# Kernel optimization log

Measured on AMD Instinct MI355X. Metric: run time of the kernel, lower is better.

Reference implementation:

```python
import jax, jax.numpy as jnp
import numpy as np

DIM = 1024
EXPAND = 2
HEAD_DIM = 64
D_STATE = 128
N_GROUPS = 1
D_CONV = 4
D_INNER = DIM * EXPAND            # 2048
N_HEADS = D_INNER // HEAD_DIM     # 32
CONV_DIM = D_INNER + 2 * N_GROUPS * D_STATE  # 2304
D_IN_PROJ = 2 * D_INNER + 2 * N_GROUPS * D_STATE + N_HEADS  # 4384
SEQLEN = 4096
LN_EPS = 1e-5


def setup_inputs() -> dict:
    key = jax.random.key(0)
    ks = jax.random.split(key, 6)
    x = jax.random.normal(ks[0], (SEQLEN, DIM), dtype=jnp.float32)
    W_in = jax.random.normal(ks[1], (D_IN_PROJ, DIM), dtype=jnp.float32) * 0.02
    conv_w = jax.random.normal(ks[2], (CONV_DIM, 1, D_CONV), dtype=jnp.float32) * 0.2
    conv_b = jax.random.normal(ks[3], (CONV_DIM,), dtype=jnp.float32) * 0.02
    # dt_bias init per module: dt ~ exp(U*(log(dt_max)-log(dt_min))+log(dt_min)); inv-softplus
    u = jax.random.uniform(ks[4], (N_HEADS,))
    dt = jnp.exp(u * (np.log(0.1) - np.log(0.001)) + np.log(0.001))
    dt = jnp.clip(dt, 1e-4)
    dt_bias = dt + jnp.log(-jnp.expm1(-dt))
    A_log = jnp.log(jax.random.uniform(ks[5], (N_HEADS,), minval=1.0, maxval=16.0))
    D = jnp.ones((N_HEADS,), dtype=jnp.float32)
    ln_w = jnp.ones((D_INNER,), dtype=jnp.float32)
    ln_b = jnp.zeros((D_INNER,), dtype=jnp.float32)
    W_out = jax.random.normal(jax.random.fold_in(key, 7), (DIM, D_INNER), dtype=jnp.float32) * 0.02
    return {"x": x, "W_in": W_in, "conv_w": conv_w, "conv_b": conv_b,
            "dt_bias": dt_bias, "A_log": A_log, "D": D,
            "ln_w": ln_w, "ln_b": ln_b, "W_out": W_out}


def _forward(x, W_in, conv_w, conv_b, dt_bias, A_log, D, ln_w, ln_b, W_out):
    L = x.shape[0]
    dtype = x.dtype
    A = -jnp.exp(A_log.astype(jnp.float32))  # (h,)
    zxbcdt = x @ W_in.T                       # (L, d_in_proj)
    z = zxbcdt[:, :D_INNER]                   # (L, d_inner)
    xbc = zxbcdt[:, D_INNER:D_INNER + CONV_DIM]
    dt = zxbcdt[:, -N_HEADS:]
    dt = jax.nn.softplus(dt.astype(jnp.float32) + dt_bias.astype(jnp.float32))  # (L, h)
    # depthwise 1D conv, SAME padding (module uses padding='SAME', then slices to L)
    xbc_c = jax.lax.conv_general_dilated(
        xbc.T[None],                          # (1, conv_dim, L)
        conv_w,                               # (conv_dim, 1, k)
        window_strides=(1,), padding='SAME',
        dimension_numbers=('NCH', 'OIH', 'NCH'),
        feature_group_count=CONV_DIM,
    )[0].T + conv_b                           # (L, conv_dim)
    xbc_s = jax.nn.silu(xbc_c)
    x_in = xbc_s[:, :D_INNER].reshape(L, N_HEADS, HEAD_DIM)      # (L, h, p)
    B = xbc_s[:, D_INNER:D_INNER + N_GROUPS * D_STATE]          # (L, n) with g=1
    C = xbc_s[:, D_INNER + N_GROUPS * D_STATE:]                 # (L, n)
    # non-causal linear attention (VSSD): y = C (B^T (x * dt * A)) + x * D
    dA = dt.astype(dtype) * A.astype(dtype)                     # (L, h)
    Vs = x_in * dA[..., None]                                   # (L, h, p)
    KV = jnp.einsum('ln,lhp->hnp', B, Vs)                       # (h, n, p)
    y = jnp.einsum('ln,hnp->lhp', C, KV) + x_in * D[None, :, None]
    y = y.reshape(L, D_INNER)
    # per-token LayerNorm, then multiplicative SiLU(z) gate
    mu = jnp.mean(y, axis=-1, keepdims=True)
    var = jnp.var(y, axis=-1, keepdims=True)
    yn = (y - mu) * jax.lax.rsqrt(var + LN_EPS) * ln_w + ln_b
    y = yn * jax.nn.silu(z)
    return y @ W_out.T                                          # (L, dim)


def reference(x, W_in, conv_w, conv_b, dt_bias, A_log, D, ln_w, ln_b, W_out):
    return _forward(x, W_in, conv_w, conv_b, dt_bias, A_log, D, ln_w, ln_b, W_out)
```

## Files before the change

### kernel.cpp

```cpp
#include <hip/hip_runtime.h>
#include <math.h>

#define SEQLEN    4096
#define DIM_IN    1024
#define D_INNER   2048
#define N_HEADS   32
#define D_STATE   128
#define CONV_DIM  2304
#define D_IN_PROJ 4384
#define PROJ_LD   4480
#define LN_EPS    1e-5f
#define KV_SPLIT  16

typedef __attribute__((ext_vector_type(8))) short bf16x8;
typedef __attribute__((ext_vector_type(4))) float f32x4;
typedef __attribute__((ext_vector_type(8))) short short8;

__device__ __forceinline__ ushort f2bf(float f) {
    union { float f; unsigned u; } v; v.f = f;
    unsigned u = v.u + 0x7FFFu + ((v.u >> 16) & 1u);
    return (ushort)(u >> 16);
}
__device__ __forceinline__ float bf2f(ushort h) {
    union { unsigned u; float f; } v; v.u = ((unsigned)h) << 16;
    return v.f;
}

__device__ __forceinline__ void gload16(const void* g, void* l) {
    __builtin_amdgcn_global_load_lds(
        (const __attribute__((address_space(1))) void*)g,
        (__attribute__((address_space(3))) void*)l, 16, 0, 0);
}

#define XB_GROUPS   (SEQLEN * DIM_IN / 8)
#define WIN_GROUPS  (PROJ_LD * DIM_IN / 8)
#define WOUT_GROUPS (DIM_IN * D_INNER / 8)
__global__ __launch_bounds__(256)
void cvt_all(const float* __restrict__ x, const float* __restrict__ W_in,
             const float* __restrict__ W_out,
             ushort* __restrict__ xb, ushort* __restrict__ Winb,
             ushort* __restrict__ Woutb) {
    int i = blockIdx.x * 256 + threadIdx.x;
    const float* src;
    ushort* dst;
    int gi;
    if (i < XB_GROUPS) {
        src = x; dst = xb; gi = i;
    } else if (i < XB_GROUPS + WIN_GROUPS) {
        gi = i - XB_GROUPS;
        int row = (gi * 8) >> 10;
        if (row >= D_IN_PROJ) {
            *reinterpret_cast<short8*>(&Winb[(size_t)gi * 8]) = (short8){0,0,0,0,0,0,0,0};
            return;
        }
        src = W_in; dst = Winb;
    } else if (i < XB_GROUPS + WIN_GROUPS + WOUT_GROUPS) {
        gi = i - (XB_GROUPS + WIN_GROUPS);
        src = W_out; dst = Woutb;
    } else return;
    float4 v0 = reinterpret_cast<const float4*>(src)[gi * 2];
    float4 v1 = reinterpret_cast<const float4*>(src)[gi * 2 + 1];
    short8 r;
    r[0] = f2bf(v0.x); r[1] = f2bf(v0.y); r[2] = f2bf(v0.z); r[3] = f2bf(v0.w);
    r[4] = f2bf(v1.x); r[5] = f2bf(v1.y); r[6] = f2bf(v1.z); r[7] = f2bf(v1.w);
    *reinterpret_cast<short8*>(&dst[(size_t)gi * 8]) = r;
}
#define CVT_TOTAL (XB_GROUPS + WIN_GROUPS + WOUT_GROUPS)

template<int NT, int NTB>
__global__ __launch_bounds__(256, 2)
void gemm_bf16_big(const ushort* __restrict__ A, int lda,
                   const ushort* __restrict__ B, int ldb,
                   ushort* __restrict__ Cout, int ldc) {
    __shared__ __align__(16) ushort S[3][12288];

    const int nwg = gridDim.x;
    const int wg  = blockIdx.x;
    const int swz = (wg & 7) * (nwg >> 3) + (wg >> 3);
    const int m0 = (swz / NTB) * 256;
    const int n0 = (swz % NTB) * 128;

    const int tid  = threadIdx.x;
    const int wave = tid >> 6;
    const int lane = tid & 63;
    const int wm = (wave >> 1) * 128;
    const int wn = (wave & 1) * 64;
    const int r16 = lane & 15;
    const int kg  = lane >> 4;
    const int pkg = kg ^ ((r16 >> 1) & 3);

    f32x4 acc[8][4];
    #pragma unroll
    for (int i = 0; i < 8; ++i)
        #pragma unroll
        for (int j = 0; j < 4; ++j) acc[i][j] = (f32x4){0.f, 0.f, 0.f, 0.f};

    const int srow = lane >> 2;
    const int scol = ((lane & 3) ^ ((lane >> 3) & 3)) * 8;
    const ushort* gsrc[6];
    #pragma unroll
    for (int i = 0; i < 6; ++i) {
        int c = wave * 6 + i;
        gsrc[i] = (c < 16)
            ? A + (size_t)(m0 + c * 16 + srow) * lda + scol
            : B + (size_t)(n0 + (c - 16) * 16 + srow) * ldb + scol;
    }

#define STAGE_BIG(T, BUF)                                            \
    {                                                                \
        const int _k = (T) * 32;                                     \
        _Pragma("unroll")                                            \
        for (int i = 0; i < 6; ++i)                                  \
            gload16(gsrc[i] + _k, &S[BUF][(wave * 6 + i) * 512]);    \
    }

    STAGE_BIG(0, 0)
    STAGE_BIG(1, 1)

    int rb = 0;
    for (int t = 0; t < NT; ++t) {
        __builtin_amdgcn_sched_barrier(0);
        if (t + 1 < NT) {
            asm volatile("s_waitcnt vmcnt(6)" ::: "memory");
        } else {
            asm volatile("s_waitcnt vmcnt(0)" ::: "memory");
        }
        __builtin_amdgcn_s_barrier();
        __builtin_amdgcn_sched_barrier(0);

        if (t + 2 < NT) {
            int sb = rb + 2; if (sb >= 3) sb -= 3;
            STAGE_BIG(t + 2, sb)
        }

        const ushort* sp = &S[rb][0];
        bf16x8 b4[4];
        #pragma unroll
        for (int ni = 0; ni < 4; ++ni)
            b4[ni] = *reinterpret_cast<const bf16x8*>(
                &sp[8192 + (wn + ni * 16 + r16) * 32 + pkg * 8]);
        #pragma unroll
        for (int mh = 0; mh < 2; ++mh) {
            bf16x8 a4[4];
            #pragma unroll
            for (int i = 0; i < 4; ++i)
                a4[i] = *reinterpret_cast<const bf16x8*>(
                    &sp[(wm + (mh * 4 + i) * 16 + r16) * 32 + pkg * 8]);
            __builtin_amdgcn_s_setprio(1);
            #pragma unroll
            for (int i = 0; i < 4; ++i)
                #pragma unroll
                for (int ni = 0; ni < 4; ++ni)
                    acc[mh * 4 + i][ni] = __builtin_amdgcn_mfma_f32_16x16x32_bf16(
                        a4[i], b4[ni], acc[mh * 4 + i][ni], 0, 0, 0);
            __builtin_amdgcn_s_setprio(0);
        }
        rb = (rb == 2) ? 0 : rb + 1;
    }
#undef STAGE_BIG

    ushort* EP = &S[0][0];
    __syncthreads();
    #pragma unroll
    for (int half = 0; half < 2; ++half) {
        if ((wave >> 1) == half) {
            #pragma unroll
            for (int mi = 0; mi < 8; ++mi)
                #pragma unroll
                for (int ni = 0; ni < 4; ++ni)
                    #pragma unroll
                    for (int r = 0; r < 4; ++r)
                        EP[(mi * 16 + kg * 4 + r) * 136 + wn + ni * 16 + r16] =
                            f2bf(acc[mi][ni][r]);
        }
        __syncthreads();
        #pragma unroll
        for (int i = 0; i < 8; ++i) {
            int idx = tid + 256 * i;
            int row = idx >> 4;
            int cb  = idx & 15;
            bf16x8 v = *reinterpret_cast<const bf16x8*>(&EP[row * 136 + cb * 8]);
            *reinterpret_cast<bf16x8*>(
                &Cout[(size_t)(m0 + half * 128 + row) * ldc + n0 + cb * 8]) = v;
        }
        __syncthreads();
    }
}

template<int BN, int NT, int OUTBF, int NTB>
__global__ __launch_bounds__(256)
void gemm_bf16_pipe(const ushort* __restrict__ A, int lda,
                    const ushort* __restrict__ B, int ldb,
                    void* __restrict__ Cout, int ldc) {
    constexpr int NI  = BN / 32;
    constexpr int BNP = BN + 8;
    __shared__ __align__(16) ushort As[3][128 * 32];
    __shared__ __align__(16) ushort Bs[3][BN * 32];

    const int nwg = gridDim.x;
    const int wg  = blockIdx.x;
    const int swz = (wg & 7) * (nwg >> 3) + (wg >> 3);
    const int m0 = (swz / NTB) * 128;
    const int n0 = (swz % NTB) * BN;

    const int tid  = threadIdx.x;
    const int wave = tid >> 6;
    const int lane = tid & 63;
    const int wm = (wave & 1) * 64;
    const int wn = (wave >> 1) * (BN / 2);
    const int r16 = lane & 15;
    const int kg  = lane >> 4;
    const int pkg = kg ^ ((r16 >> 1) & 3);

    f32x4 acc[4][NI];
    #pragma unroll
    for (int i = 0; i < 4; ++i)
        #pragma unroll
        for (int j = 0; j < NI; ++j) acc[i][j] = (f32x4){0.f, 0.f, 0.f, 0.f};

    const int srow = lane >> 2;
    const int scol = ((lane & 3) ^ ((lane >> 3) & 3)) * 8;
    const int ca0 = wave * 2, ca1 = wave * 2 + 1;
    const ushort* gA0 = A + (size_t)(m0 + ca0 * 16 + srow) * lda + scol;
    const ushort* gA1 = A + (size_t)(m0 + ca1 * 16 + srow) * lda + scol;
    const ushort* gB0;
    const ushort* gB1 = nullptr;
    int cb0, cb1 = 0;
    if constexpr (BN == 128) {
        cb0 = wave * 2; cb1 = wave * 2 + 1;
        gB0 = B + (size_t)(n0 + cb0 * 16 + srow) * ldb + scol;
        gB1 = B + (size_t)(n0 + cb1 * 16 + srow) * ldb + scol;
    } else {
        cb0 = wave;
        gB0 = B + (size_t)(n0 + cb0 * 16 + srow) * ldb + scol;
    }

#define STAGE_STEP(T, BUF)                                          \
    {                                                               \
        const int _k = (T) * 32;                                    \
        gload16(gA0 + _k, &As[BUF][ca0 * 512]);                     \
        gload16(gA1 + _k, &As[BUF][ca1 * 512]);                     \
        gload16(gB0 + _k, &Bs[BUF][cb0 * 512]);                     \
        if constexpr (BN == 128) gload16(gB1 + _k, &Bs[BUF][cb1 * 512]); \
    }

    STAGE_STEP(0, 0)
    STAGE_STEP(1, 1)

    int rb = 0;
    for (int t = 0; t < NT; ++t) {
        __builtin_amdgcn_sched_barrier(0);
        if (t + 1 < NT) {
            if constexpr (BN == 128) asm volatile("s_waitcnt vmcnt(4)" ::: "memory");
            else                     asm volatile("s_waitcnt vmcnt(3)" ::: "memory");
        } else {
            asm volatile("s_waitcnt vmcnt(0)" ::: "memory");
        }
        __builtin_amdgcn_s_barrier();
        __builtin_amdgcn_sched_barrier(0);

        if (t + 2 < NT) {
            int sb = rb + 2; if (sb >= 3) sb -= 3;
            STAGE_STEP(t + 2, sb)
        }

        const ushort* ab = &As[rb][0];
        const ushort* bb = &Bs[rb][0];
        bf16x8 a[4], b[NI];
        #pragma unroll
        for (int mi = 0; mi < 4; ++mi)
            a[mi] = *reinterpret_cast<const bf16x8*>(&ab[(wm + mi * 16 + r16) * 32 + pkg * 8]);
        #pragma unroll
        for (int ni = 0; ni < NI; ++ni)
            b[ni] = *reinterpret_cast<const bf16x8*>(&bb[(wn + ni * 16 + r16) * 32 + pkg * 8]);

        __builtin_amdgcn_s_setprio(1);
        #pragma unroll
        for (int mi = 0; mi < 4; ++mi)
            #pragma unroll
            for (int ni = 0; ni < NI; ++ni)
                acc[mi][ni] = __builtin_amdgcn_mfma_f32_16x16x32_bf16(a[mi], b[ni], acc[mi][ni], 0, 0, 0);
        __builtin_amdgcn_s_setprio(0);

        rb = (rb == 2) ? 0 : rb + 1;
    }
#undef STAGE_STEP

    if constexpr (OUTBF) {
        ushort* EP = &As[0][0];
        ushort* outp = (ushort*)Cout;
        __syncthreads();
        #pragma unroll
        for (int half = 0; half < 2; ++half) {
            if ((wave & 1) == half) {
                #pragma unroll
                for (int mi = 0; mi < 4; ++mi)
                    #pragma unroll
                    for (int ni = 0; ni < NI; ++ni)
                        #pragma unroll
                        for (int r = 0; r < 4; ++r)
                            EP[(mi * 16 + kg * 4 + r) * BNP + wn + ni * 16 + r16] =
                                f2bf(acc[mi][ni][r]);
            }
            __syncthreads();
            #pragma unroll
            for (int i = 0; i < BN / 32; ++i) {
                int idx = tid + 256 * i;
                int row = idx / (BN / 8);
                int cb  = idx % (BN / 8);
                bf16x8 v = *reinterpret_cast<const bf16x8*>(&EP[row * BNP + cb * 8]);
                *reinterpret_cast<bf16x8*>(
                    &outp[(size_t)(m0 + half * 64 + row) * ldc + n0 + cb * 8]) = v;
            }
            __syncthreads();
        }
    } else {
        float* outp = (float*)Cout;
        #pragma unroll
        for (int mi = 0; mi < 4; ++mi)
            #pragma unroll
            for (int ni = 0; ni < NI; ++ni)
                #pragma unroll
                for (int r = 0; r < 4; ++r) {
                    int row = m0 + wm + mi * 16 + kg * 4 + r;
                    int col = n0 + wn + ni * 16 + r16;
                    outp[(size_t)row * ldc + col] = acc[mi][ni][r];
                }
    }
}

__global__ __launch_bounds__(256)
void conv_silu_kernel(const ushort* __restrict__ zxb,
                      const float* __restrict__ conv_w,
                      const float* __restrict__ conv_b,
                      const float* __restrict__ dt_bias,
                      const float* __restrict__ A_log,
                      ushort* __restrict__ xbcs,
                      float* __restrict__ dA) {
    const int l = blockIdx.x;
    const ushort* base = zxb + (size_t)l * PROJ_LD + D_INNER;
    const short8 zero8 = (short8){0,0,0,0,0,0,0,0};
    for (int g = threadIdx.x; g < CONV_DIM / 8; g += 256) {
        const int c = g * 8;
        short8 xm = (l >= 1)
            ? *reinterpret_cast<const short8*>(base + c - PROJ_LD) : zero8;
        short8 x0 = *reinterpret_cast<const short8*>(base + c);
        short8 xp = (l + 1 < SEQLEN)
            ? *reinterpret_cast<const short8*>(base + c + PROJ_LD) : zero8;
        short8 xq = (l + 2 < SEQLEN)
            ? *reinterpret_cast<const short8*>(base + c + 2 * PROJ_LD) : zero8;
        float4 bia0 = *reinterpret_cast<const float4*>(&conv_b[c]);
        float4 bia1 = *reinterpret_cast<const float4*>(&conv_b[c + 4]);
        const float* bp = &bia0.x;
        short8 o;
        #pragma unroll
        for (int j = 0; j < 8; ++j) {
            float4 w = *reinterpret_cast<const float4*>(&conv_w[(c + j) * 4]);
            float acc = (j < 4 ? (&bia0.x)[j] : (&bia1.x)[j - 4]);
            acc += w.x * bf2f((ushort)xm[j]);
            acc += w.y * bf2f((ushort)x0[j]);
            acc += w.z * bf2f((ushort)xp[j]);
            acc += w.w * bf2f((ushort)xq[j]);
            float s = acc / (1.0f + expf(-acc));
            o[j] = f2bf(s);
        }
        (void)bp;
        *reinterpret_cast<short8*>(&xbcs[(size_t)l * CONV_DIM + c]) = o;
    }
    if (threadIdx.x < N_HEADS) {
        int h = threadIdx.x;
        float v = bf2f(zxb[(size_t)l * PROJ_LD + (D_IN_PROJ - N_HEADS) + h]) + dt_bias[h];
        float sp = (v > 20.0f) ? v : log1pf(expf(v));
        dA[l * N_HEADS + h] = sp * (-expf(A_log[h]));
    }
}

__global__ __launch_bounds__(256)
void kv_kernel(const ushort* __restrict__ xbcs,
               const float* __restrict__ dA,
               float* __restrict__ KVp) {
    __shared__ float Vs[16][132];
    __shared__ float Bsm[16][132];
    const int hp0 = blockIdx.x * 128;
    const int lc0 = blockIdx.y * (SEQLEN / KV_SPLIT);
    const int tid = threadIdx.x;
    const int ty = tid >> 4, tx = tid & 15;
    float acc[8][8];
    #pragma unroll
    for (int i = 0; i < 8; ++i)
        #pragma unroll
        for (int j = 0; j < 8; ++j) acc[i][j] = 0.0f;

    for (int ls = 0; ls < SEQLEN / KV_SPLIT; ls += 16) {
        {
            int lrow = tid >> 4;
            int p8   = (tid & 15) * 8;
            int l = lc0 + ls + lrow;
            short8 v = *reinterpret_cast<const short8*>(
                &xbcs[(size_t)l * CONV_DIM + hp0 + p8]);
            float a = dA[l * N_HEADS + ((hp0 + p8) >> 6)];
            #pragma unroll
            for (int j = 0; j < 8; ++j) Vs[lrow][p8 + j] = bf2f((ushort)v[j]) * a;
            short8 b = *reinterpret_cast<const short8*>(
                &xbcs[(size_t)l * CONV_DIM + D_INNER + p8]);
            #pragma unroll
            for (int j = 0; j < 8; ++j) Bsm[lrow][p8 + j] = bf2f((ushort)b[j]);
        }
        __syncthreads();
        #pragma unroll
        for (int k = 0; k < 16; ++k) {
            float a[8], b[8];
            *reinterpret_cast<float4*>(&a[0]) = *reinterpret_cast<const float4*>(&Vs[k][ty * 8]);
            *reinterpret_cast<float4*>(&a[4]) = *reinterpret_cast<const float4*>(&Vs[k][ty * 8 + 4]);
            *reinterpret_cast<float4*>(&b[0]) = *reinterpret_cast<const float4*>(&Bsm[k][tx * 8]);
            *reinterpret_cast<float4*>(&b[4]) = *reinterpret_cast<const float4*>(&Bsm[k][tx * 8 + 4]);
            #pragma unroll
            for (int i = 0; i < 8; ++i)
                #pragma unroll
                for (int j = 0; j < 8; ++j)
                    acc[i][j] = fmaf(a[i], b[j], acc[i][j]);
        }
        __syncthreads();
    }
    float* dst = KVp + (size_t)blockIdx.y * (D_INNER * D_STATE);
    #pragma unroll
    for (int i = 0; i < 8; ++i) {
        int hp = hp0 + ty * 8 + i;
        #pragma unroll
        for (int j = 0; j < 8; j += 4) {
            float4 v = make_float4(acc[i][j], acc[i][j+1], acc[i][j+2], acc[i][j+3]);
            *reinterpret_cast<float4*>(&dst[(size_t)hp * D_STATE + tx * 8 + j]) = v;
        }
    }
}

__global__ __launch_bounds__(256)
void kv_reduce(const float* __restrict__ KVp, ushort* __restrict__ KVTb) {
    int i = blockIdx.x * 256 + threadIdx.x;
    float4 s = make_float4(0.f, 0.f, 0.f, 0.f);
    #pragma unroll
    for (int c = 0; c < KV_SPLIT; ++c) {
        float4 v = reinterpret_cast<const float4*>(KVp + (size_t)c * (D_INNER * D_STATE))[i];
        s.x += v.x; s.y += v.y; s.z += v.z; s.w += v.w;
    }
    ushort4 o;
    o.x = f2bf(s.x); o.y = f2bf(s.y); o.z = f2bf(s.z); o.w = f2bf(s.w);
    *reinterpret_cast<ushort4*>(&KVTb[i * 4]) = o;
}

__global__ __launch_bounds__(256)
void ln_gate_kernel(const ushort* __restrict__ y1b,
                    const ushort* __restrict__ xbcs,
                    const ushort* __restrict__ zxb,
                    const float* __restrict__ Dp,
                    const float* __restrict__ ln_w,
                    const float* __restrict__ ln_b,
                    ushort* __restrict__ yb) {
    const int l = blockIdx.x;
    const int tid = threadIdx.x;
    const int c = tid * 8;
    float y[8], z[8];
    float sum = 0.f, sumsq = 0.f;
    {
        short8 v  = *reinterpret_cast<const short8*>(&y1b[(size_t)l * D_INNER + c]);
        short8 xi = *reinterpret_cast<const short8*>(&xbcs[(size_t)l * CONV_DIM + c]);
        short8 zz = *reinterpret_cast<const short8*>(&zxb[(size_t)l * PROJ_LD + c]);
        float d = Dp[c >> 6];
        #pragma unroll
        for (int j = 0; j < 8; ++j) {
            float yv = bf2f((ushort)v[j]) + bf2f((ushort)xi[j]) * d;
            y[j] = yv;
            z[j] = bf2f((ushort)zz[j]);
            sum += yv;
            sumsq += yv * yv;
        }
    }
    #pragma unroll
    for (int off = 32; off > 0; off >>= 1) {
        sum   += __shfl_down(sum, off);
        sumsq += __shfl_down(sumsq, off);
    }
    __shared__ float red[8];
    int wid = tid >> 6;
    if ((tid & 63) == 0) { red[wid] = sum; red[4 + wid] = sumsq; }
    __syncthreads();
    sum   = red[0] + red[1] + red[2] + red[3];
    sumsq = red[4] + red[5] + red[6] + red[7];
    float mu  = sum * (1.0f / D_INNER);
    float var = sumsq * (1.0f / D_INNER) - mu * mu;
    float rs  = rsqrtf(var + LN_EPS);
    short8 o;
    #pragma unroll
    for (int j = 0; j < 8; ++j) {
        float yn = (y[j] - mu) * rs * ln_w[c + j] + ln_b[c + j];
        float g  = z[j] / (1.0f + expf(-z[j]));
        o[j] = f2bf(yn * g);
    }
    *reinterpret_cast<short8*>(&yb[(size_t)l * D_INNER + c]) = o;
}

extern "C" void kernel_launch(void* const* d_in, const int* in_sizes, int n_in,
                              void* d_out, int out_size, void* d_ws, size_t ws_size,
                              hipStream_t stream) {
    const float* x       = (const float*)d_in[0];
    const float* W_in    = (const float*)d_in[1];
    const float* conv_w  = (const float*)d_in[2];
    const float* conv_b  = (const float*)d_in[3];
    const float* dt_bias = (const float*)d_in[4];
    const float* A_log   = (const float*)d_in[5];
    const float* Dp      = (const float*)d_in[6];
    const float* ln_w    = (const float*)d_in[7];
    const float* ln_b    = (const float*)d_in[8];
    const float* W_out   = (const float*)d_in[9];
    float* out = (float*)d_out;

    char* ws = (char*)d_ws;
    ushort* zxb   = (ushort*)ws;
    ushort* xbcs  = (ushort*)(ws +  36700160);
    ushort* y1b   = (ushort*)(ws +  55574528);
    ushort* yb    = (ushort*)(ws +  72351744);
    float*  KVp   = (float*)(ws +  89128960);
    float*  dA    = (float*)(ws + 105906176);
    ushort* KVTb  = (ushort*)(ws + 106430464);
    ushort* Woutb = (ushort*)(ws + 106954752);
    ushort* xb    = (ushort*)(ws + 111149056);
    ushort* Winb  = (ushort*)(ws + 119537664);

    cvt_all<<<(CVT_TOTAL + 255) / 256, 256, 0, stream>>>(x, W_in, W_out, xb, Winb, Woutb);

    gemm_bf16_big<32, 35><<<16 * (PROJ_LD / 128), 256, 0, stream>>>(
        xb, DIM_IN, Winb, DIM_IN, zxb, PROJ_LD);

    conv_silu_kernel<<<SEQLEN, 256, 0, stream>>>(zxb, conv_w, conv_b, dt_bias, A_log,
                                                 xbcs, dA);

    kv_kernel<<<dim3(16, KV_SPLIT), 256, 0, stream>>>(xbcs, dA, KVp);
    kv_reduce<<<(D_INNER * D_STATE / 4) / 256, 256, 0, stream>>>(KVp, KVTb);

    gemm_bf16_pipe<128, 4, 1, 16><<<(D_INNER / 128) * 32, 256, 0, stream>>>(
        xbcs + (D_INNER + D_STATE), CONV_DIM, KVTb, D_STATE, y1b, D_INNER);

    ln_gate_kernel<<<SEQLEN, 256, 0, stream>>>(y1b, xbcs, zxb, Dp, ln_w, ln_b, yb);

    gemm_bf16_pipe<64, 64, 0, 16><<<(DIM_IN / 64) * 32, 256, 0, stream>>>(
        yb, D_INNER, Woutb, D_INNER, out, DIM_IN);
}
```

Measured before the change: 199.4 us.

## Use 512-thread blocks with 8 waves in the input-projection GEMM

Result: no change. 196.2 us (-1.6%).

```diff
diff --git a/kernel.cpp b/kernel.cpp
--- a/kernel.cpp
+++ b/kernel.cpp
@@ -68,7 +68,7 @@
 #define CVT_TOTAL (XB_GROUPS + WIN_GROUPS + WOUT_GROUPS)
 
 template<int NT, int NTB>
-__global__ __launch_bounds__(256, 2)
+__global__ __launch_bounds__(512, 4)
 void gemm_bf16_big(const ushort* __restrict__ A, int lda,
                    const ushort* __restrict__ B, int ldb,
                    ushort* __restrict__ Cout, int ldc) {
@@ -83,24 +83,24 @@
     const int tid  = threadIdx.x;
     const int wave = tid >> 6;
     const int lane = tid & 63;
-    const int wm = (wave >> 1) * 128;
-    const int wn = (wave & 1) * 64;
+    const int wr = wave >> 1;
+    const int wc = wave & 1;
     const int r16 = lane & 15;
     const int kg  = lane >> 4;
     const int pkg = kg ^ ((r16 >> 1) & 3);
 
-    f32x4 acc[8][4];
-    #pragma unroll
-    for (int i = 0; i < 8; ++i)
+    f32x4 acc[4][4];
+    #pragma unroll
+    for (int i = 0; i < 4; ++i)
         #pragma unroll
         for (int j = 0; j < 4; ++j) acc[i][j] = (f32x4){0.f, 0.f, 0.f, 0.f};
 
     const int srow = lane >> 2;
     const int scol = ((lane & 3) ^ ((lane >> 3) & 3)) * 8;
-    const ushort* gsrc[6];
-    #pragma unroll
-    for (int i = 0; i < 6; ++i) {
-        int c = wave * 6 + i;
+    const ushort* gsrc[3];
+    #pragma unroll
+    for (int i = 0; i < 3; ++i) {
+        int c = wave * 3 + i;
         gsrc[i] = (c < 16)
             ? A + (size_t)(m0 + c * 16 + srow) * lda + scol
             : B + (size_t)(n0 + (c - 16) * 16 + srow) * ldb + scol;
@@ -110,8 +110,8 @@
     {                                                                \
         const int _k = (T) * 32;                                     \
         _Pragma("unroll")                                            \
-        for (int i = 0; i < 6; ++i)                                  \
-            gload16(gsrc[i] + _k, &S[BUF][(wave * 6 + i) * 512]);    \
+        for (int i = 0; i < 3; ++i)                                  \
+            gload16(gsrc[i] + _k, &S[BUF][(wave * 3 + i) * 512]);    \
     }
 
     STAGE_BIG(0, 0)
@@ -121,7 +121,7 @@
     for (int t = 0; t < NT; ++t) {
         __builtin_amdgcn_sched_barrier(0);
         if (t + 1 < NT) {
-            asm volatile("s_waitcnt vmcnt(6)" ::: "memory");
+            asm volatile("s_waitcnt vmcnt(3)" ::: "memory");
         } else {
             asm volatile("s_waitcnt vmcnt(0)" ::: "memory");
         }
@@ -134,27 +134,24 @@
         }
 
         const ushort* sp = &S[rb][0];
-        bf16x8 b4[4];
+        bf16x8 a4[4], b4[4];
         #pragma unroll
         for (int ni = 0; ni < 4; ++ni)
             b4[ni] = *reinterpret_cast<const bf16x8*>(
-                &sp[8192 + (wn + ni * 16 + r16) * 32 + pkg * 8]);
-        #pragma unroll
-        for (int mh = 0; mh < 2; ++mh) {
-            bf16x8 a4[4];
-            #pragma unroll
-            for (int i = 0; i < 4; ++i)
-                a4[i] = *reinterpret_cast<const bf16x8*>(
-                    &sp[(wm + (mh * 4 + i) * 16 + r16) * 32 + pkg * 8]);
-            __builtin_amdgcn_s_setprio(1);
-            #pragma unroll
-            for (int i = 0; i < 4; ++i)
-                #pragma unroll
-                for (int ni = 0; ni < 4; ++ni)
-                    acc[mh * 4 + i][ni] = __builtin_amdgcn_mfma_f32_16x16x32_bf16(
-                        a4[i], b4[ni], acc[mh * 4 + i][ni], 0, 0, 0);
-            __builtin_amdgcn_s_setprio(0);
-        }
+                &sp[8192 + (wc * 64 + ni * 16 + r16) * 32 + pkg * 8]);
+        #pragma unroll
+        for (int mi = 0; mi < 4; ++mi)
+            a4[mi] = *reinterpret_cast<const bf16x8*>(
+                &sp[(wr * 64 + mi * 16 + r16) * 32 + pkg * 8]);
+        __builtin_amdgcn_s_setprio(1);
+        #pragma unroll
+        for (int mi = 0; mi < 4; ++mi)
+            #pragma unroll
+            for (int ni = 0; ni < 4; ++ni)
+                acc[mi][ni] = __builtin_amdgcn_mfma_f32_16x16x32_bf16(
+                    a4[mi], b4[ni], acc[mi][ni], 0, 0, 0);
+        __builtin_amdgcn_s_setprio(0);
+
         rb = (rb == 2) ? 0 : rb + 1;
     }
 #undef STAGE_BIG
@@ -162,28 +159,22 @@
     ushort* EP = &S[0][0];
     __syncthreads();
     #pragma unroll
-    for (int half = 0; half < 2; ++half) {
-        if ((wave >> 1) == half) {
-            #pragma unroll
-            for (int mi = 0; mi < 8; ++mi)
-                #pragma unroll
-                for (int ni = 0; ni < 4; ++ni)
-                    #pragma unroll
-                    for (int r = 0; r < 4; ++r)
-                        EP[(mi * 16 + kg * 4 + r) * 136 + wn + ni * 16 + r16] =
-                            f2bf(acc[mi][ni][r]);
-        }
-        __syncthreads();
-        #pragma unroll
-        for (int i = 0; i < 8; ++i) {
-            int idx = tid + 256 * i;
-            int row = idx >> 4;
-            int cb  = idx & 15;
-            bf16x8 v = *reinterpret_cast<const bf16x8*>(&EP[row * 136 + cb * 8]);
-            *reinterpret_cast<bf16x8*>(
-                &Cout[(size_t)(m0 + half * 128 + row) * ldc + n0 + cb * 8]) = v;
-        }
-        __syncthreads();
+    for (int mi = 0; mi < 4; ++mi)
+        #pragma unroll
+        for (int ni = 0; ni < 4; ++ni)
+            #pragma unroll
+            for (int r = 0; r < 4; ++r)
+                EP[(wr * 64 + mi * 16 + kg * 4 + r) * 136 + wc * 64 + ni * 16 + r16] =
+                    f2bf(acc[mi][ni][r]);
+    __syncthreads();
+    #pragma unroll
+    for (int i = 0; i < 8; ++i) {
+        int idx = tid + 512 * i;
+        int row = idx >> 4;
+        int cb  = idx & 15;
+        bf16x8 v = *reinterpret_cast<const bf16x8*>(&EP[row * 136 + cb * 8]);
+        *reinterpret_cast<bf16x8*>(
+            &Cout[(size_t)(m0 + row) * ldc + n0 + cb * 8]) = v;
     }
 }
 
@@ -351,7 +342,6 @@
             ? *reinterpret_cast<const short8*>(base + c + 2 * PROJ_LD) : zero8;
         float4 bia0 = *reinterpret_cast<const float4*>(&conv_b[c]);
         float4 bia1 = *reinterpret_cast<const float4*>(&conv_b[c + 4]);
-        const float* bp = &bia0.x;
         short8 o;
         #pragma unroll
         for (int j = 0; j < 8; ++j) {
@@ -364,7 +354,6 @@
             float s = acc / (1.0f + expf(-acc));
             o[j] = f2bf(s);
         }
-        (void)bp;
         *reinterpret_cast<short8*>(&xbcs[(size_t)l * CONV_DIM + c]) = o;
     }
     if (threadIdx.x < N_HEADS) {
@@ -528,7 +517,7 @@
 
     cvt_all<<<(CVT_TOTAL + 255) / 256, 256, 0, stream>>>(x, W_in, W_out, xb, Winb, Woutb);
 
-    gemm_bf16_big<32, 35><<<16 * (PROJ_LD / 128), 256, 0, stream>>>(
+    gemm_bf16_big<32, 35><<<16 * (PROJ_LD / 128), 512, 0, stream>>>(
         xb, DIM_IN, Winb, DIM_IN, zxb, PROJ_LD);
 
     conv_silu_kernel<<<SEQLEN, 256, 0, stream>>>(zxb, conv_w, conv_b, dt_bias, A_log,
```
